# Optimization experiments

Hardware: AMD Instinct MI355X
Metric: run time of the kernel (lower is better)

The kernel has to match this reference:

```python
import jax, jax.numpy as jnp
import numpy as np

T, B, D, L = 4096, 64, 128, 128

def setup_inputs() -> dict:
    key = jax.random.key(0)
    k1, k2, k3 = jax.random.split(key, 3)
    scale_x = 1.0 / np.sqrt(D)
    scale_h = 1.0 / np.sqrt(L)
    return {
        "x": jax.random.normal(k1, (T, B, D), dtype=jnp.float32),
        "h": jnp.zeros((B, L), dtype=jnp.float32),
        "Wx": jax.random.normal(k2, (D, L), dtype=jnp.float32) * scale_x,
        "bx": jnp.zeros((L,), dtype=jnp.float32),
        "Wh": jax.random.normal(k3, (L, L), dtype=jnp.float32) * scale_h,
        "bh": jnp.zeros((L,), dtype=jnp.float32),
    }

def reference(x, h, Wx, bx, Wh, bh):
    # Batch the input projection across all timesteps (one big GEMM),
    # then scan the recurrent projection + tanh across time.
    xp = jnp.einsum('tbd,dl->tbl', x, Wx) + bx  # [T,B,L]

    def step(h_prev, x_t):
        h_new = jnp.tanh(x_t + h_prev @ Wh + bh)  # [B,L]
        return h_new, h_new

    _, H = jax.lax.scan(step, h, xp)
    return H  # [T,B,L]
```

## Files before the change

kernel.cpp:

```cpp
#include <hip/hip_runtime.h>

#define T_ 4096
#define B_ 64
#define D_ 128
#define L_ 128

__global__ __launch_bounds__(256, 3) void xp_gemm(
    const float* __restrict__ x, const float* __restrict__ Wx,
    const float* __restrict__ bx, float* __restrict__ xp)
{
  __shared__ float sX[64][132];
  __shared__ float sW[32][132];
  const int j = threadIdx.x;
  const int m0 = blockIdx.x * 64;

#pragma unroll
  for (int r = 0; r < 8; ++r) {
    int f = r * 256 + j;
    int row = f >> 5, k4 = f & 31;
    float4 v = *reinterpret_cast<const float4*>(x + (size_t)(m0 + row) * 128 + k4 * 4);
    *reinterpret_cast<float4*>(&sX[row][k4 * 4]) = v;
  }
#pragma unroll
  for (int r = 0; r < 4; ++r) {
    int f = r * 256 + j;
    int row = f >> 5, c4 = f & 31;
    float4 v = *reinterpret_cast<const float4*>(Wx + (size_t)row * 128 + c4 * 4);
    *reinterpret_cast<float4*>(&sW[row][c4 * 4]) = v;
  }
  __syncthreads();

  const int rr = j >> 4;
  const int cc = j & 15;
  const int c0 = cc * 4;
  const int c1 = 64 + cc * 4;
  float a0[4][4], a1[4][4];
  float4 b0 = *reinterpret_cast<const float4*>(bx + c0);
  float4 b1 = *reinterpret_cast<const float4*>(bx + c1);
#pragma unroll
  for (int i2 = 0; i2 < 4; ++i2) {
    a0[i2][0] = b0.x; a0[i2][1] = b0.y; a0[i2][2] = b0.z; a0[i2][3] = b0.w;
    a1[i2][0] = b1.x; a1[i2][1] = b1.y; a1[i2][2] = b1.z; a1[i2][3] = b1.w;
  }

  for (int ch = 0; ch < 4; ++ch) {
#pragma unroll 2
    for (int k4 = 0; k4 < 8; ++k4) {
      float4 xv[4];
#pragma unroll
      for (int i2 = 0; i2 < 4; ++i2)
        xv[i2] = *reinterpret_cast<const float4*>(&sX[rr * 4 + i2][ch * 32 + k4 * 4]);
#pragma unroll
      for (int dk = 0; dk < 4; ++dk) {
        float4 w0 = *reinterpret_cast<const float4*>(&sW[k4 * 4 + dk][c0]);
        float4 w1 = *reinterpret_cast<const float4*>(&sW[k4 * 4 + dk][c1]);
#pragma unroll
        for (int i2 = 0; i2 < 4; ++i2) {
          float xs = (dk == 0) ? xv[i2].x : (dk == 1) ? xv[i2].y
                   : (dk == 2) ? xv[i2].z : xv[i2].w;
          a0[i2][0] = fmaf(xs, w0.x, a0[i2][0]);
          a0[i2][1] = fmaf(xs, w0.y, a0[i2][1]);
          a0[i2][2] = fmaf(xs, w0.z, a0[i2][2]);
          a0[i2][3] = fmaf(xs, w0.w, a0[i2][3]);
          a1[i2][0] = fmaf(xs, w1.x, a1[i2][0]);
          a1[i2][1] = fmaf(xs, w1.y, a1[i2][1]);
          a1[i2][2] = fmaf(xs, w1.z, a1[i2][2]);
          a1[i2][3] = fmaf(xs, w1.w, a1[i2][3]);
        }
      }
    }
    if (ch < 3) {
      __syncthreads();
#pragma unroll
      for (int r = 0; r < 4; ++r) {
        int f = r * 256 + j;
        int row = f >> 5, c4 = f & 31;
        float4 v = *reinterpret_cast<const float4*>(
            Wx + (size_t)((ch + 1) * 32 + row) * 128 + c4 * 4);
        *reinterpret_cast<float4*>(&sW[row][c4 * 4]) = v;
      }
      __syncthreads();
    }
  }

#pragma unroll
  for (int i2 = 0; i2 < 4; ++i2) {
    float* p = xp + (size_t)(m0 + rr * 4 + i2) * 128;
    float4 o0 = {a0[i2][0], a0[i2][1], a0[i2][2], a0[i2][3]};
    float4 o1 = {a1[i2][0], a1[i2][1], a1[i2][2], a1[i2][3]};
    *reinterpret_cast<float4*>(p + c0) = o0;
    *reinterpret_cast<float4*>(p + c1) = o1;
  }
}

__global__ __launch_bounds__(512, 1) void rnn_scan(
    float* io, const float* __restrict__ h0,
    const float* __restrict__ Wh, const float* __restrict__ bh)
{
  __shared__ float hbuf[2][128];
  const int j = threadIdx.x;
  const int b = blockIdx.x;
  const int i = j & 63;
  const int l = ((j >> 6) << 4) | (i >> 2);
  const int kh = i & 3;
  const int kb = kh << 5;

  float wh[32];
#pragma unroll
  for (int m = 0; m < 8; ++m) {
    int ku = (m + 2 * kh) & 7;
#pragma unroll
    for (int e = 0; e < 4; ++e)
      wh[4 * m + e] = Wh[(size_t)(kb + ku * 4 + e) * 128 + l];
  }
  const float bhr = bh[l];

  if (j < 128) hbuf[0][j] = h0[(size_t)b * 128 + j];

  const size_t ss = (size_t)B_ * L_;
  const float* __restrict__ pf = io + (size_t)b * 128 + l;
  float* outp = io + (size_t)b * 128 + l;

  float q[8];
#pragma unroll
  for (int u = 0; u < 8; ++u) q[u] = pf[u * ss];
  pf += 8 * ss;

  __syncthreads();

  for (int t8 = 0; t8 < T_ / 8; ++t8) {
#pragma unroll
    for (int u = 0; u < 8; ++u) {
      const int t = (t8 << 3) + u;
      const int pr = u & 1;
      const float* hb = &hbuf[pr][kb];

      float c0 = 0.f, c1 = 0.f, c2 = 0.f, c3 = 0.f;
#pragma unroll
      for (int m = 0; m < 8; ++m) {
        int ku = (m + 2 * kh) & 7;
        float4 hv = *reinterpret_cast<const float4*>(hb + ku * 4);
        float acc = (m & 3) == 0 ? c0 : (m & 3) == 1 ? c1 : (m & 3) == 2 ? c2 : c3;
        acc = fmaf(hv.x, wh[4 * m + 0], acc);
        acc = fmaf(hv.y, wh[4 * m + 1], acc);
        acc = fmaf(hv.z, wh[4 * m + 2], acc);
        acc = fmaf(hv.w, wh[4 * m + 3], acc);
        if ((m & 3) == 0) c0 = acc; else if ((m & 3) == 1) c1 = acc;
        else if ((m & 3) == 2) c2 = acc; else c3 = acc;
      }
      float acc = (c0 + c1) + (c2 + c3);
      acc += __shfl_xor(acc, 1, 64);
      acc += __shfl_xor(acc, 2, 64);
      float pre = acc + q[u] + bhr;

      float aa = fabsf(pre);
      float e2 = __expf(-2.f * aa);
      float r = (1.f - e2) * __builtin_amdgcn_rcpf(1.f + e2);
      float hn = copysignf(r, pre);

      if (kh == 0) hbuf[pr ^ 1][l] = hn;
      else if (kh == 3) outp[(size_t)t * ss] = hn;

      q[u] = (t + 8 < T_) ? pf[0] : 0.f;
      pf += ss;

      asm volatile("s_waitcnt lgkmcnt(0)" ::: "memory");
      __builtin_amdgcn_s_barrier();
      __builtin_amdgcn_sched_barrier(0);
    }
  }
}

extern "C" void kernel_launch(void* const* d_in, const int* in_sizes, int n_in,
                              void* d_out, int out_size, void* d_ws, size_t ws_size,
                              hipStream_t stream) {
  const float* x  = (const float*)d_in[0];
  const float* h0 = (const float*)d_in[1];
  const float* Wx = (const float*)d_in[2];
  const float* bx = (const float*)d_in[3];
  const float* Wh = (const float*)d_in[4];
  const float* bh = (const float*)d_in[5];
  float* out = (float*)d_out;

  xp_gemm<<<(T_ * B_) / 64, 256, 0, stream>>>(x, Wx, bx, out);
  rnn_scan<<<B_, 512, 0, stream>>>(out, h0, Wh, bh);
}
```

Baseline: 1.830 ms.

## Fuse input projection GEMM into recurrent scan kernel with double-buffered x tiles

```diff
diff --git a/kernel.cpp b/kernel.cpp
--- a/kernel.cpp
+++ b/kernel.cpp
@@ -5,164 +5,94 @@
 #define D_ 128
 #define L_ 128
 
-__global__ __launch_bounds__(256, 3) void xp_gemm(
-    const float* __restrict__ x, const float* __restrict__ Wx,
-    const float* __restrict__ bx, float* __restrict__ xp)
+__global__ __launch_bounds__(256, 1) void rnn_fused(
+    const float* __restrict__ x, const float* __restrict__ h0,
+    const float* __restrict__ Wx, const float* __restrict__ bx,
+    const float* __restrict__ Wh, const float* __restrict__ bh,
+    float* __restrict__ out)
 {
-  __shared__ float sX[64][132];
-  __shared__ float sW[32][132];
+  __shared__ float hbuf[2][128];
+  __shared__ float xtile[2][8][128];
+
   const int j = threadIdx.x;
-  const int m0 = blockIdx.x * 64;
+  const int b = blockIdx.x;
+  const int half = j & 1;
+  const int l = j >> 1;
+  const int kb = half << 6;
 
+  float wh[64], wx[64];
 #pragma unroll
-  for (int r = 0; r < 8; ++r) {
-    int f = r * 256 + j;
-    int row = f >> 5, k4 = f & 31;
-    float4 v = *reinterpret_cast<const float4*>(x + (size_t)(m0 + row) * 128 + k4 * 4);
-    *reinterpret_cast<float4*>(&sX[row][k4 * 4]) = v;
+  for (int kk = 0; kk < 64; ++kk) {
+    wh[kk] = Wh[(size_t)(kb + kk) * L_ + l];
+    wx[kk] = Wx[(size_t)(kb + kk) * L_ + l];
   }
-#pragma unroll
-  for (int r = 0; r < 4; ++r) {
-    int f = r * 256 + j;
-    int row = f >> 5, c4 = f & 31;
-    float4 v = *reinterpret_cast<const float4*>(Wx + (size_t)row * 128 + c4 * 4);
-    *reinterpret_cast<float4*>(&sW[row][c4 * 4]) = v;
+  const float bias = bh[l] + bx[l];
+
+  if (j < 128) hbuf[0][j] = h0[(size_t)b * L_ + j];
+
+  {
+    int r = j >> 5, c4 = (j & 31) * 4;
+    float4 v = *reinterpret_cast<const float4*>(x + ((size_t)r * B_ + b) * D_ + c4);
+    *reinterpret_cast<float4*>(&xtile[0][r][c4]) = v;
+  }
+  float4 gx;
+  {
+    int r = 8 + (j >> 5), c4 = (j & 31) * 4;
+    gx = *reinterpret_cast<const float4*>(x + ((size_t)r * B_ + b) * D_ + c4);
   }
   __syncthreads();
 
-  const int rr = j >> 4;
-  const int cc = j & 15;
-  const int c0 = cc * 4;
-  const int c1 = 64 + cc * 4;
-  float a0[4][4], a1[4][4];
-  float4 b0 = *reinterpret_cast<const float4*>(bx + c0);
-  float4 b1 = *reinterpret_cast<const float4*>(bx + c1);
-#pragma unroll
-  for (int i2 = 0; i2 < 4; ++i2) {
-    a0[i2][0] = b0.x; a0[i2][1] = b0.y; a0[i2][2] = b0.z; a0[i2][3] = b0.w;
-    a1[i2][0] = b1.x; a1[i2][1] = b1.y; a1[i2][2] = b1.z; a1[i2][3] = b1.w;
-  }
-
-  for (int ch = 0; ch < 4; ++ch) {
-#pragma unroll 2
-    for (int k4 = 0; k4 < 8; ++k4) {
-      float4 xv[4];
-#pragma unroll
-      for (int i2 = 0; i2 < 4; ++i2)
-        xv[i2] = *reinterpret_cast<const float4*>(&sX[rr * 4 + i2][ch * 32 + k4 * 4]);
-#pragma unroll
-      for (int dk = 0; dk < 4; ++dk) {
-        float4 w0 = *reinterpret_cast<const float4*>(&sW[k4 * 4 + dk][c0]);
-        float4 w1 = *reinterpret_cast<const float4*>(&sW[k4 * 4 + dk][c1]);
-#pragma unroll
-        for (int i2 = 0; i2 < 4; ++i2) {
-          float xs = (dk == 0) ? xv[i2].x : (dk == 1) ? xv[i2].y
-                   : (dk == 2) ? xv[i2].z : xv[i2].w;
-          a0[i2][0] = fmaf(xs, w0.x, a0[i2][0]);
-          a0[i2][1] = fmaf(xs, w0.y, a0[i2][1]);
-          a0[i2][2] = fmaf(xs, w0.z, a0[i2][2]);
-          a0[i2][3] = fmaf(xs, w0.w, a0[i2][3]);
-          a1[i2][0] = fmaf(xs, w1.x, a1[i2][0]);
-          a1[i2][1] = fmaf(xs, w1.y, a1[i2][1]);
-          a1[i2][2] = fmaf(xs, w1.z, a1[i2][2]);
-          a1[i2][3] = fmaf(xs, w1.w, a1[i2][3]);
-        }
-      }
-    }
-    if (ch < 3) {
-      __syncthreads();
-#pragma unroll
-      for (int r = 0; r < 4; ++r) {
-        int f = r * 256 + j;
-        int row = f >> 5, c4 = f & 31;
-        float4 v = *reinterpret_cast<const float4*>(
-            Wx + (size_t)((ch + 1) * 32 + row) * 128 + c4 * 4);
-        *reinterpret_cast<float4*>(&sW[row][c4 * 4]) = v;
-      }
-      __syncthreads();
-    }
-  }
-
-#pragma unroll
-  for (int i2 = 0; i2 < 4; ++i2) {
-    float* p = xp + (size_t)(m0 + rr * 4 + i2) * 128;
-    float4 o0 = {a0[i2][0], a0[i2][1], a0[i2][2], a0[i2][3]};
-    float4 o1 = {a1[i2][0], a1[i2][1], a1[i2][2], a1[i2][3]};
-    *reinterpret_cast<float4*>(p + c0) = o0;
-    *reinterpret_cast<float4*>(p + c1) = o1;
-  }
-}
-
-__global__ __launch_bounds__(512, 1) void rnn_scan(
-    float* io, const float* __restrict__ h0,
-    const float* __restrict__ Wh, const float* __restrict__ bh)
-{
-  __shared__ float hbuf[2][128];
-  const int j = threadIdx.x;
-  const int b = blockIdx.x;
-  const int i = j & 63;
-  const int l = ((j >> 6) << 4) | (i >> 2);
-  const int kh = i & 3;
-  const int kb = kh << 5;
-
-  float wh[32];
-#pragma unroll
-  for (int m = 0; m < 8; ++m) {
-    int ku = (m + 2 * kh) & 7;
-#pragma unroll
-    for (int e = 0; e < 4; ++e)
-      wh[4 * m + e] = Wh[(size_t)(kb + ku * 4 + e) * 128 + l];
-  }
-  const float bhr = bh[l];
-
-  if (j < 128) hbuf[0][j] = h0[(size_t)b * 128 + j];
-
   const size_t ss = (size_t)B_ * L_;
-  const float* __restrict__ pf = io + (size_t)b * 128 + l;
-  float* outp = io + (size_t)b * 128 + l;
-
-  float q[8];
-#pragma unroll
-  for (int u = 0; u < 8; ++u) q[u] = pf[u * ss];
-  pf += 8 * ss;
-
-  __syncthreads();
+  float* outp = out + (size_t)b * L_ + l;
 
   for (int t8 = 0; t8 < T_ / 8; ++t8) {
+    const int cur = t8 & 1;
 #pragma unroll
     for (int u = 0; u < 8; ++u) {
-      const int t = (t8 << 3) + u;
       const int pr = u & 1;
-      const float* hb = &hbuf[pr][kb];
 
-      float c0 = 0.f, c1 = 0.f, c2 = 0.f, c3 = 0.f;
+      if (u == 1) {
+        int r = j >> 5, c4 = (j & 31) * 4;
+        *reinterpret_cast<float4*>(&xtile[cur ^ 1][r][c4]) = gx;
+      }
+      if (u == 4) {
+        int rr = (t8 + 2) * 8 + (j >> 5);
+        if (rr > T_ - 1) rr = T_ - 1;
+        int c4 = (j & 31) * 4;
+        gx = *reinterpret_cast<const float4*>(x + ((size_t)rr * B_ + b) * D_ + c4);
+      }
+
+      const float* xr = &xtile[cur][u][kb];
+      const float* hr = &hbuf[pr][kb];
+      float a0 = 0.f, a1 = 0.f, a2 = 0.f, a3 = 0.f;
 #pragma unroll
-      for (int m = 0; m < 8; ++m) {
-        int ku = (m + 2 * kh) & 7;
-        float4 hv = *reinterpret_cast<const float4*>(hb + ku * 4);
-        float acc = (m & 3) == 0 ? c0 : (m & 3) == 1 ? c1 : (m & 3) == 2 ? c2 : c3;
-        acc = fmaf(hv.x, wh[4 * m + 0], acc);
-        acc = fmaf(hv.y, wh[4 * m + 1], acc);
-        acc = fmaf(hv.z, wh[4 * m + 2], acc);
-        acc = fmaf(hv.w, wh[4 * m + 3], acc);
-        if ((m & 3) == 0) c0 = acc; else if ((m & 3) == 1) c1 = acc;
-        else if ((m & 3) == 2) c2 = acc; else c3 = acc;
+      for (int m = 0; m < 16; ++m) {
+        float4 xv = *reinterpret_cast<const float4*>(xr + m * 4);
+        a0 = fmaf(xv.x, wx[4 * m + 0], a0);
+        a1 = fmaf(xv.y, wx[4 * m + 1], a1);
+        a2 = fmaf(xv.z, wx[4 * m + 2], a2);
+        a3 = fmaf(xv.w, wx[4 * m + 3], a3);
       }
-      float acc = (c0 + c1) + (c2 + c3);
-      acc += __shfl_xor(acc, 1, 64);
-      acc += __shfl_xor(acc, 2, 64);
-      float pre = acc + q[u] + bhr;
+#pragma unroll
+      for (int m = 0; m < 16; ++m) {
+        float4 hv = *reinterpret_cast<const float4*>(hr + m * 4);
+        a0 = fmaf(hv.x, wh[4 * m + 0], a0);
+        a1 = fmaf(hv.y, wh[4 * m + 1], a1);
+        a2 = fmaf(hv.z, wh[4 * m + 2], a2);
+        a3 = fmaf(hv.w, wh[4 * m + 3], a3);
+      }
+      float part = (a0 + a1) + (a2 + a3);
+      float sum = part + __shfl_xor(part, 1, 64);
+      float pre = sum + bias;
 
       float aa = fabsf(pre);
       float e2 = __expf(-2.f * aa);
-      float r = (1.f - e2) * __builtin_amdgcn_rcpf(1.f + e2);
-      float hn = copysignf(r, pre);
+      float r1 = (1.f - e2) * __builtin_amdgcn_rcpf(1.f + e2);
+      float hn = copysignf(r1, pre);
 
-      if (kh == 0) hbuf[pr ^ 1][l] = hn;
-      else if (kh == 3) outp[(size_t)t * ss] = hn;
-
-      q[u] = (t + 8 < T_) ? pf[0] : 0.f;
-      pf += ss;
+      if (half == 0) hbuf[pr ^ 1][l] = hn;
+      else           *outp = hn;
+      outp += ss;
 
       asm volatile("s_waitcnt lgkmcnt(0)" ::: "memory");
       __builtin_amdgcn_s_barrier();
@@ -182,6 +112,5 @@
   const float* bh = (const float*)d_in[5];
   float* out = (float*)d_out;
 
-  xp_gemm<<<(T_ * B_) / 64, 256, 0, stream>>>(x, Wx, bx, out);
-  rnn_scan<<<B_, 512, 0, stream>>>(out, h0, Wh, bh);
+  rnn_fused<<<B_, 256, 0, stream>>>(x, h0, Wx, bx, Wh, bh, out);
 }
```

Result: slower. 2.997 ms (+63.8%).
